# Kernel optimization log

Measured on AMD Instinct MI355X. Metric: run time of the kernel, lower is better.

## Reference

```python
import jax, jax.numpy as jnp
import numpy as np

N_NODES, N_EDGES, D_IN, N_GRAPHS = 20000, 320000, 256, 32
H1, C1, H2, C2 = 4, 128, 4, 64


def setup_inputs() -> dict:
    key = jax.random.key(0)
    ks = jax.random.split(key, 24)
    g = lambda k, shape, fan: jax.random.normal(k, shape, jnp.float32) * (1.0 / np.sqrt(fan))
    inp = {
        'x': jax.random.normal(ks[0], (N_NODES, D_IN), jnp.float32),
        'edge_index': jax.random.randint(ks[1], (2, N_EDGES), 0, N_NODES, jnp.int32),
        'batch': jnp.sort(jax.random.randint(ks[2], (N_NODES,), 0, N_GRAPHS, jnp.int32)),
        'edge_attr': jax.random.normal(ks[3], (N_EDGES, 1), jnp.float32),
        # GATConv 1: lin [D_IN, H1*C1], att_src/dst/edge [H1,C1], lin_edge [1,H1*C1], bias [H1*C1]
        'W1': g(ks[4], (D_IN, H1 * C1), D_IN),
        'as1': g(ks[5], (H1, C1), C1),
        'ad1': g(ks[6], (H1, C1), C1),
        'We1': g(ks[7], (1, H1 * C1), 1),
        'ae1': g(ks[8], (H1, C1), C1),
        'b1': jnp.zeros((H1 * C1,), jnp.float32),
        'g1': jnp.ones((H1 * C1,), jnp.float32),
        'be1': jnp.zeros((H1 * C1,), jnp.float32),
        # GATConv 2 (concat=False -> out 64)
        'W2': g(ks[9], (H1 * C1, H2 * C2), H1 * C1),
        'as2': g(ks[10], (H2, C2), C2),
        'ad2': g(ks[11], (H2, C2), C2),
        'We2': g(ks[12], (1, H2 * C2), 1),
        'ae2': g(ks[13], (H2, C2), C2),
        'b2': jnp.zeros((C2,), jnp.float32),
        'g2': jnp.ones((C2,), jnp.float32),
        'be2': jnp.zeros((C2,), jnp.float32),
        'fw1': g(ks[14], (C2, 32), C2),
        'fb1': jnp.zeros((32,), jnp.float32),
        'fw2': g(ks[15], (32, 1), 32),
        'fb2': jnp.zeros((1,), jnp.float32),
    }
    return inp


def _gat(x, src, dst, ea, W, a_s, a_d, We, a_e, bias, H, C, concat, n):
    h = (x @ W).reshape(n, H, C)                         # [N,H,C]
    al_s = jnp.einsum('nhc,hc->nh', h, a_s)              # [N,H]
    al_d = jnp.einsum('nhc,hc->nh', h, a_d)
    e = (ea @ We).reshape(-1, H, C)                      # [E',H,C]
    al_e = jnp.einsum('ehc,hc->eh', e, a_e)
    logits = jax.nn.leaky_relu(al_s[src] + al_d[dst] + al_e, 0.2)  # [E',H]
    m = jax.ops.segment_max(logits, dst, num_segments=n)
    m = jnp.where(jnp.isfinite(m), m, 0.0)
    p = jnp.exp(logits - m[dst])
    denom = jax.ops.segment_sum(p, dst, num_segments=n)
    alpha = p / (denom[dst] + 1e-16)                     # segment softmax
    out = jax.ops.segment_sum(h[src] * alpha[:, :, None], dst, num_segments=n)
    out = out.reshape(n, H * C) if concat else out.mean(axis=1)
    return out + bias


def _bn(x, gamma, beta):
    mu = x.mean(axis=0)
    var = x.var(axis=0)
    return gamma * (x - mu) * jax.lax.rsqrt(var + 1e-5) + beta


def reference(x, edge_index, batch, edge_attr, W1, as1, ad1, We1, ae1, b1, g1, be1,
              W2, as2, ad2, We2, ae2, b2, g2, be2, fw1, fb1, fw2, fb2):
    n = x.shape[0]
    loop = jnp.arange(n, dtype=edge_index.dtype)
    src = jnp.concatenate([edge_index[0], loop])
    dst = jnp.concatenate([edge_index[1], loop])
    # self-loop edge_attr filled with mean (PyG fill_value='mean')
    ea = jnp.concatenate([edge_attr, jnp.broadcast_to(edge_attr.mean(axis=0), (n, edge_attr.shape[1]))])

    h = _gat(x, src, dst, ea, W1, as1, ad1, We1, ae1, b1, H1, C1, True, n)
    h = jax.nn.elu(_bn(h, g1, be1))
    h = _gat(h, src, dst, ea, W2, as2, ad2, We2, ae2, b2, H2, C2, False, n)
    h = jax.nn.elu(_bn(h, g2, be2))

    sums = jax.ops.segment_sum(h, batch, num_segments=N_GRAPHS)
    cnt = jax.ops.segment_sum(jnp.ones((n,), h.dtype), batch, num_segments=N_GRAPHS)
    pooled = sums / jnp.maximum(cnt, 1.0)[:, None]       # global_mean_pool
    # dropout is identity in eval mode
    out = jax.nn.elu(pooled @ fw1 + fb1) @ fw2 + fb2
    return out
```

## Files before the change

### kernel.cpp

```cpp
#include <hip/hip_runtime.h>
#include <hip/hip_bf16.h>

#define N_NODES  20000
#define MPAD     20096
#define N_EDGES  320000
#define N_EP     (N_EDGES + N_NODES)
#define D_IN     256
#define N_GRAPHS 32
#define HH1 4
#define CC1 128
#define HH2 4
#define CC2 64

#define XB_OFF      0ull
#define HB1_OFF     10289152ull
#define AGG1_OFF    30867456ull
#define HB2_OFF     51445760ull
#define OUT2_OFF    61734912ull
#define ALPHA_OFF   66854912ull
#define DENOM_OFF   72294912ull
#define EAF_OFF     72614912ull
#define W1BT_OFF    73894912ull
#define W2BT_OFF    74157056ull
#define CSR_OFF     74419200ull
#define ROWPTR_OFF  77139200ull
#define GSTART_OFF  77219264ull
#define SMALL_OFF   77219520ull
#define SBUF_OFF    77245120ull
#define EAP_OFF     77245184ull
#define ALSP_OFF    77246464ull
#define ALDP_OFF    77889536ull
#define ALS1_OFF    78532608ull
#define ALD1_OFF    78854144ull
#define ALS2_OFF    79175680ull
#define ALD2_OFF    79497216ull
#define PMU1_OFF    79818752ull
#define PM21_OFF    80343040ull
#define PMU2_OFF    80867328ull
#define PM22_OFF    80932864ull
#define MUSUM1_OFF  80998400ull
#define M2SUM1_OFF  81000448ull
#define MUSUM2_OFF  81002496ull
#define M2SUM2_OFF  81003008ull
#define EAACC_OFF   81003520ull
#define DEG_OFF     81003584ull
#define CURS_OFF    81083584ull
#define FLAGZ_OFF   81163584ull
#define ZERO0_START DEG_OFF
#define ZERO0_SIZE  160128ull

#define S_AS1 0
#define S_AD1 512
#define S_WE1 1024
#define S_AE1 1536
#define S_G1  2048
#define S_BE1 2560
#define S_AS2 3072
#define S_AD2 3328
#define S_WE2 3584
#define S_AE2 3840
#define S_G2  4096
#define S_BE2 4160
#define S_FW1 4224
#define S_FB1 6272
#define S_FW2 6304
#define S_FB2 6336

typedef __attribute__((ext_vector_type(8))) short bf8_t;
typedef __attribute__((ext_vector_type(4))) float f4_t;

__global__ void detect_dtype(const unsigned short* __restrict__ xr, int* __restrict__ flag) {
    int i = blockIdx.x * blockDim.x + threadIdx.x;
    unsigned short u = xr[i];
    if ((u & 0x7F80) == 0x7F80) atomicOr(flag, 1);
}

__device__ __forceinline__ float loadF(const void* p, int i, int fp32) {
    return fp32 ? ((const float*)p)[i]
                : __bfloat162float(((const __hip_bfloat16*)p)[i]);
}

#define PB_XB  5024
#define PB_EAF 313
#define PB_W   512
#define PB_SM  16
#define PREP_BLOCKS (PB_XB + PB_EAF + 2 * PB_W + PB_SM + 1)
__global__ __launch_bounds__(256) void prep(
        const int* __restrict__ flag,
        const void* x, const void* ea, const void* W1, const void* W2,
        const void* as1, const void* ad1, const void* We1, const void* ae1,
        const void* g1, const void* be1, const void* as2, const void* ad2,
        const void* We2, const void* ae2, const void* g2, const void* be2,
        const void* fw1, const void* fb1, const void* fw2, const void* fb2,
        __hip_bfloat16* __restrict__ xb, float* __restrict__ eaf, float* __restrict__ eap,
        __hip_bfloat16* __restrict__ W1bt, __hip_bfloat16* __restrict__ W2bt,
        float* __restrict__ smalls, float* __restrict__ sbuf) {
    __shared__ float sh[256];
    int b = blockIdx.x, t = threadIdx.x;
    int fp32 = flag[0];
    if (b < PB_XB) {
        int base = (b * 256 + t) * 4;
        __hip_bfloat16 tmp[4];
#pragma unroll
        for (int j = 0; j < 4; ++j) {
            int i = base + j;
            float v = (i < N_NODES * D_IN) ? loadF(x, i, fp32) : 0.f;
            tmp[j] = __float2bfloat16(v);
        }
        *(uint2*)&xb[base] = *(uint2*)tmp;
        return;
    }
    b -= PB_XB;
    if (b < PB_EAF) {
        int base = (b * 256 + t) * 4;
        float s = 0.f;
#pragma unroll
        for (int j = 0; j < 4; ++j) {
            int i = base + j;
            if (i < N_EDGES) { float v = loadF(ea, i, fp32); eaf[i] = v; s += v; }
        }
        sh[t] = s;
        __syncthreads();
        for (int st = 128; st; st >>= 1) {
            if (t < st) sh[t] += sh[t + st];
            __syncthreads();
        }
        if (t == 0) eap[b] = sh[0];
        return;
    }
    b -= PB_EAF;
    if (b < PB_W) {
        int i = b * 256 + t;
        int k = i >> 9, n = i & 511;
        W1bt[(size_t)n * 256 + k] = __float2bfloat16(loadF(W1, i, fp32));
        return;
    }
    b -= PB_W;
    if (b < PB_W) {
        int i = b * 256 + t;
        int k = i >> 8, n = i & 255;
        W2bt[(size_t)n * 512 + k] = __float2bfloat16(loadF(W2, i, fp32));
        return;
    }
    b -= PB_W;
    if (b < PB_SM) {
        const void* srcs[16] = {as1, ad1, We1, ae1, g1, be1, as2, ad2, We2, ae2, g2, be2, fw1, fb1, fw2, fb2};
        const int cnts[16] = {512, 512, 512, 512, 512, 512, 256, 256, 256, 256, 64, 64, 2048, 32, 32, 1};
        const int offs[16] = {S_AS1, S_AD1, S_WE1, S_AE1, S_G1, S_BE1, S_AS2, S_AD2,
                              S_WE2, S_AE2, S_G2, S_BE2, S_FW1, S_FB1, S_FW2, S_FB2};
        for (int i = t; i < cnts[b]; i += 256)
            smalls[offs[b] + i] = loadF(srcs[b], i, fp32);
        return;
    }
    if (t < 4) {
        float s = 0.f;
        for (int c = 0; c < CC1; ++c) s += loadF(We1, t * CC1 + c, fp32) * loadF(ae1, t * CC1 + c, fp32);
        sbuf[t] = s;
    } else if (t < 8) {
        int h = t - 4;
        float s = 0.f;
        for (int c = 0; c < CC2; ++c) s += loadF(We2, h * CC2 + c, fp32) * loadF(ae2, h * CC2 + c, fp32);
        sbuf[4 + h] = s;
    }
}

#define HIST_BLOCKS 1329
__global__ void hist_bounds(const int* __restrict__ ei, int* __restrict__ deg,
                            const int* __restrict__ batch, int* __restrict__ gstart) {
    int b = blockIdx.x, t = threadIdx.x;
    if (b < HIST_BLOCKS) {
        int e = b * 256 + t;
        if (e >= N_EP) return;
        int d = (e < N_EDGES) ? ei[N_EDGES + e] : e - N_EDGES;
        atomicAdd(&deg[d], 1);
        return;
    }
    int i = (b - HIST_BLOCKS) * 256 + t;
    if (i >= N_NODES) return;
    int bb = batch[i];
    if (i == 0) {
        for (int g = 0; g <= bb; ++g) gstart[g] = 0;
    } else {
        int pb = batch[i - 1];
        for (int g = pb + 1; g <= bb; ++g) gstart[g] = i;
    }
    if (i == N_NODES - 1) {
        for (int g = bb + 1; g <= N_GRAPHS; ++g) gstart[g] = N_NODES;
    }
}

__global__ __launch_bounds__(1024) void deg_scan(const int* __restrict__ deg, int* __restrict__ rowptr,
                                                 const float* __restrict__ eap, float* __restrict__ ea_acc) {
    __shared__ int part[1024];
    int t = threadIdx.x;
    int lo = t * 20;
    int hi = lo + 20; if (hi > N_NODES) hi = N_NODES; if (lo > N_NODES) lo = N_NODES;
    int s = 0;
    for (int i = lo; i < hi; ++i) s += deg[i];
    part[t] = s;
    __syncthreads();
    for (int off = 1; off < 1024; off <<= 1) {
        int u = (t >= off) ? part[t - off] : 0;
        __syncthreads();
        if (t >= off) part[t] += u;
        __syncthreads();
    }
    int run = part[t] - s;
    for (int i = lo; i < hi; ++i) { rowptr[i] = run; run += deg[i]; }
    if (hi == N_NODES && lo < N_NODES) rowptr[N_NODES] = run;
    if (t == 0) {
        float es = 0.f;
        for (int i = 0; i < PB_EAF; ++i) es += eap[i];
        ea_acc[0] = es;
    }
}

__global__ void edge_scatter(const int* __restrict__ ei, const int* __restrict__ rowptr,
                             int* __restrict__ cursor, int2* __restrict__ csr_se) {
    int e = blockIdx.x * blockDim.x + threadIdx.x;
    if (e >= N_EP) return;
    int s, d;
    if (e < N_EDGES) { s = ei[e]; d = ei[N_EDGES + e]; }
    else { s = d = e - N_EDGES; }
    int pos = rowptr[d] + atomicAdd(&cursor[d], 1);
    csr_se[pos] = make_int2(s, e);
}

__global__ __launch_bounds__(64) void csr_sort(const int* __restrict__ rowptr, int2* __restrict__ cs) {
    __shared__ int2 buf[128];
    int d = blockIdx.x;
    int beg = rowptr[d], end = rowptr[d + 1], n = end - beg;
    int lane = threadIdx.x;
    if (n <= 1) return;
    if (n <= 128) {
        for (int i = lane; i < n; i += 64) buf[i] = cs[beg + i];
        __syncthreads();
        if (lane == 0) {
            for (int i = 1; i < n; ++i) {
                int2 key = buf[i]; int j = i - 1;
                while (j >= 0 && buf[j].y > key.y) { buf[j + 1] = buf[j]; --j; }
                buf[j + 1] = key;
            }
        }
        __syncthreads();
        for (int i = lane; i < n; i += 64) cs[beg + i] = buf[i];
    } else if (lane == 0) {
        for (int i = beg + 1; i < end; ++i) {
            int2 key = cs[i]; int j = i - 1;
            while (j >= beg && cs[j].y > key.y) { cs[j + 1] = cs[j]; --j; }
            cs[j + 1] = key;
        }
    }
}

__global__ __launch_bounds__(256) void gemm_mfma_al(
        const short* __restrict__ A, const short* __restrict__ Bt,
        __hip_bfloat16* __restrict__ Cb, int N, int K,
        float* __restrict__ alsp, float* __restrict__ aldp,
        const float* __restrict__ asv, const float* __restrict__ adv, int cshift) {
    __shared__ short As[128 * 40];
    __shared__ short Bs[64 * 40];
    int t = threadIdx.x;
    int wv = t >> 6, lane = t & 63, quad = lane >> 4, lr = lane & 15;
    int m0 = blockIdx.y * 128, n0 = blockIdx.x * 64;
    f4_t acc[2][4] = {};
    int ra0 = t >> 2, sa0 = t & 3;
    int ra1 = (t + 256) >> 2;
    for (int k0 = 0; k0 < K; k0 += 32) {
        *(uint4*)&As[ra0 * 40 + sa0 * 8] = *(const uint4*)&A[(size_t)(m0 + ra0) * K + k0 + sa0 * 8];
        *(uint4*)&As[ra1 * 40 + sa0 * 8] = *(const uint4*)&A[(size_t)(m0 + ra1) * K + k0 + sa0 * 8];
        *(uint4*)&Bs[ra0 * 40 + sa0 * 8] = *(const uint4*)&Bt[(size_t)(n0 + ra0) * K + k0 + sa0 * 8];
        __syncthreads();
        bf8_t a0 = *(const bf8_t*)&As[(wv * 16 + lr) * 40 + quad * 8];
        bf8_t a1 = *(const bf8_t*)&As[((wv + 4) * 16 + lr) * 40 + quad * 8];
#pragma unroll
        for (int nt = 0; nt < 4; ++nt) {
            bf8_t b = *(const bf8_t*)&Bs[(nt * 16 + lr) * 40 + quad * 8];
            acc[0][nt] = __builtin_amdgcn_mfma_f32_16x16x32_bf16(a0, b, acc[0][nt], 0, 0, 0);
            acc[1][nt] = __builtin_amdgcn_mfma_f32_16x16x32_bf16(a1, b, acc[1][nt], 0, 0, 0);
        }
        __syncthreads();
    }
#pragma unroll
    for (int si = 0; si < 2; ++si) {
        int mrow = m0 + (wv + si * 4) * 16 + quad * 4;
#pragma unroll
        for (int nt = 0; nt < 4; ++nt) {
            int col = n0 + nt * 16 + lr;
#pragma unroll
            for (int r = 0; r < 4; ++r)
                Cb[(size_t)(mrow + r) * N + col] = __float2bfloat16(acc[si][nt][r]);
        }
    }
    float asv4[4], adv4[4];
#pragma unroll
    for (int nt = 0; nt < 4; ++nt) {
        asv4[nt] = asv[n0 + nt * 16 + lr];
        adv4[nt] = adv[n0 + nt * 16 + lr];
    }
    int hsel = n0 >> cshift;
    int parity = (n0 >> 6) & ((1 << (cshift - 6)) - 1);
#pragma unroll
    for (int si = 0; si < 2; ++si) {
#pragma unroll
        for (int r = 0; r < 4; ++r) {
            float ps = 0.f, pd = 0.f;
#pragma unroll
            for (int nt = 0; nt < 4; ++nt) {
                ps += acc[si][nt][r] * asv4[nt];
                pd += acc[si][nt][r] * adv4[nt];
            }
#pragma unroll
            for (int m = 1; m < 16; m <<= 1) {
                ps += __shfl_xor(ps, m);
                pd += __shfl_xor(pd, m);
            }
            if (lr == 0) {
                int row = m0 + (wv + si * 4) * 16 + quad * 4 + r;
                alsp[(row * 4 + hsel) * 2 + parity] = ps;
                aldp[(row * 4 + hsel) * 2 + parity] = pd;
            }
        }
    }
}

__global__ void al_combine(const float* __restrict__ alsp, const float* __restrict__ aldp,
                           float* __restrict__ als, float* __restrict__ ald, int nparts) {
    int i = blockIdx.x * blockDim.x + threadIdx.x;
    if (i >= MPAD * 4) return;
    float s = alsp[2 * i], d0 = aldp[2 * i];
    if (nparts == 2) { s += alsp[2 * i + 1]; d0 += aldp[2 * i + 1]; }
    als[i] = s; ald[i] = d0;
}

__global__ __launch_bounds__(64) void edge_softmax_csr(
        const int* __restrict__ rowptr, const int2* __restrict__ csr_se,
        const float* __restrict__ als, const float* __restrict__ ald,
        const float* __restrict__ eaf, const float* __restrict__ ea_acc,
        const float* __restrict__ sbuf, float* __restrict__ alpha, float* __restrict__ denom) {
    int d = blockIdx.x;
    int lane = threadIdx.x;
    int beg = rowptr[d], end = rowptr[d + 1];
    float ea_mean = ea_acc[0] * (1.0f / N_EDGES);
    float4 ad = *(const float4*)&ald[d * 4];
    float s0 = sbuf[0], s1 = sbuf[1], s2 = sbuf[2], s3 = sbuf[3];
    float m0 = -INFINITY, m1 = -INFINITY, m2 = -INFINITY, m3 = -INFINITY;
    for (int p = beg + lane; p < end; p += 64) {
        int2 se = csr_se[p];
        float eav = (se.y < N_EDGES) ? eaf[se.y] : ea_mean;
        float4 as = *(const float4*)&als[se.x * 4];
        float l0 = as.x + ad.x + eav * s0; l0 = l0 > 0.f ? l0 : 0.2f * l0;
        float l1 = as.y + ad.y + eav * s1; l1 = l1 > 0.f ? l1 : 0.2f * l1;
        float l2 = as.z + ad.z + eav * s2; l2 = l2 > 0.f ? l2 : 0.2f * l2;
        float l3 = as.w + ad.w + eav * s3; l3 = l3 > 0.f ? l3 : 0.2f * l3;
        float4 lv = {l0, l1, l2, l3};
        *(float4*)&alpha[(size_t)p * 4] = lv;
        m0 = fmaxf(m0, l0); m1 = fmaxf(m1, l1); m2 = fmaxf(m2, l2); m3 = fmaxf(m3, l3);
    }
#pragma unroll
    for (int off = 1; off < 64; off <<= 1) {
        m0 = fmaxf(m0, __shfl_xor(m0, off));
        m1 = fmaxf(m1, __shfl_xor(m1, off));
        m2 = fmaxf(m2, __shfl_xor(m2, off));
        m3 = fmaxf(m3, __shfl_xor(m3, off));
    }
    float t0 = 0.f, t1 = 0.f, t2 = 0.f, t3 = 0.f;
    for (int p = beg + lane; p < end; p += 64) {
        float4 lv = *(const float4*)&alpha[(size_t)p * 4];
        lv.x = __expf(lv.x - m0); lv.y = __expf(lv.y - m1);
        lv.z = __expf(lv.z - m2); lv.w = __expf(lv.w - m3);
        *(float4*)&alpha[(size_t)p * 4] = lv;
        t0 += lv.x; t1 += lv.y; t2 += lv.z; t3 += lv.w;
    }
#pragma unroll
    for (int off = 1; off < 64; off <<= 1) {
        t0 += __shfl_xor(t0, off);
        t1 += __shfl_xor(t1, off);
        t2 += __shfl_xor(t2, off);
        t3 += __shfl_xor(t3, off);
    }
    if (lane == 0) {
        float4 dn = {t0, t1, t2, t3};
        *(float4*)&denom[d * 4] = dn;
    }
}

__global__ __launch_bounds__(128) void agg1_csr(
        const int* __restrict__ rowptr, const int2* __restrict__ csr_se,
        const float* __restrict__ alpha, const float* __restrict__ denom,
        const __hip_bfloat16* __restrict__ hb, __hip_bfloat16* __restrict__ outb) {
    int d = blockIdx.x;
    int t = threadIdx.x;
    int h = t >> 5;
    float rdn = 1.0f / (denom[d * 4 + h] + 1e-16f);
    float a0 = 0.f, a1 = 0.f, a2 = 0.f, a3 = 0.f;
    int beg = rowptr[d], end = rowptr[d + 1];
    for (int p = beg; p < end; ++p) {
        int2 se = csr_se[p];
        float w = alpha[(size_t)p * 4 + h];
        uint2 raw = *(const uint2*)&hb[(size_t)se.x * 512 + 4 * t];
        a0 += w * __uint_as_float(raw.x << 16);
        a1 += w * __uint_as_float(raw.x & 0xFFFF0000u);
        a2 += w * __uint_as_float(raw.y << 16);
        a3 += w * __uint_as_float(raw.y & 0xFFFF0000u);
    }
    __hip_bfloat16 tmp[4] = {__float2bfloat16(a0 * rdn), __float2bfloat16(a1 * rdn),
                             __float2bfloat16(a2 * rdn), __float2bfloat16(a3 * rdn)};
    *(uint2*)&outb[(size_t)d * 512 + 4 * t] = *(uint2*)tmp;
}

__global__ __launch_bounds__(64) void agg2_hm(
        const int* __restrict__ rowptr, const int2* __restrict__ csr_se,
        const float* __restrict__ alpha, const float* __restrict__ denom,
        const __hip_bfloat16* __restrict__ hb, float* __restrict__ out2) {
    int d = blockIdx.x;
    int t = threadIdx.x;
    int h = t >> 4;
    float rdn = 1.0f / (denom[d * 4 + h] + 1e-16f);
    float a0 = 0.f, a1 = 0.f, a2 = 0.f, a3 = 0.f;
    int beg = rowptr[d], end = rowptr[d + 1];
    for (int p = beg; p < end; ++p) {
        int2 se = csr_se[p];
        float w = alpha[(size_t)p * 4 + h];
        uint2 raw = *(const uint2*)&hb[(size_t)se.x * 256 + 4 * t];
        a0 += w * __uint_as_float(raw.x << 16);
        a1 += w * __uint_as_float(raw.x & 0xFFFF0000u);
        a2 += w * __uint_as_float(raw.y << 16);
        a3 += w * __uint_as_float(raw.y & 0xFFFF0000u);
    }
    __shared__ float sh[256];
    sh[4 * t] = a0 * rdn; sh[4 * t + 1] = a1 * rdn;
    sh[4 * t + 2] = a2 * rdn; sh[4 * t + 3] = a3 * rdn;
    __syncthreads();
    if (t < 16) {
        float4 v;
        v.x = 0.25f * (sh[4 * t] + sh[64 + 4 * t] + sh[128 + 4 * t] + sh[192 + 4 * t]);
        v.y = 0.25f * (sh[4 * t + 1] + sh[64 + 4 * t + 1] + sh[128 + 4 * t + 1] + sh[192 + 4 * t + 1]);
        v.z = 0.25f * (sh[4 * t + 2] + sh[64 + 4 * t + 2] + sh[128 + 4 * t + 2] + sh[192 + 4 * t + 2]);
        v.w = 0.25f * (sh[4 * t + 3] + sh[64 + 4 * t + 3] + sh[128 + 4 * t + 3] + sh[192 + 4 * t + 3]);
        *(float4*)&out2[(size_t)d * 64 + 4 * t] = v;
    }
}

__global__ __launch_bounds__(256) void bn_part_b(const __hip_bfloat16* __restrict__ x,
                                                 float* __restrict__ pmu, float* __restrict__ pm2) {
    int t = threadIdx.x, b = blockIdx.x;
    float s0 = 0.f, s20 = 0.f, s1 = 0.f, s21 = 0.f;
    for (int i = b; i < N_NODES; i += gridDim.x) {
        unsigned u = *(const unsigned*)&x[(size_t)i * 512 + 2 * t];
        float v0 = __uint_as_float(u << 16);
        float v1 = __uint_as_float(u & 0xFFFF0000u);
        s0 += v0; s20 += v0 * v0; s1 += v1; s21 += v1 * v1;
    }
    pmu[b * 512 + 2 * t] = s0;     pm2[b * 512 + 2 * t] = s20;
    pmu[b * 512 + 2 * t + 1] = s1; pm2[b * 512 + 2 * t + 1] = s21;
}

__global__ void bn_reduce(const float* __restrict__ pmu, const float* __restrict__ pm2,
                          float* __restrict__ musum, float* __restrict__ m2sum, int nch) {
    int c = blockIdx.x * blockDim.x + threadIdx.x;
    if (c >= nch) return;
    float s = 0.f, s2 = 0.f;
    for (int b = 0; b < 256; ++b) { s += pmu[b * nch + c]; s2 += pm2[b * nch + c]; }
    musum[c] = s; m2sum[c] = s2;
}

__global__ __launch_bounds__(256) void bn_apply_elu_b16(__hip_bfloat16* __restrict__ x,
                                                        const float* __restrict__ musum,
                                                        const float* __restrict__ m2sum,
                                                        const float* __restrict__ smalls) {
    int q = blockIdx.x * blockDim.x + threadIdx.x;
    if (q >= N_NODES * 512 / 4) return;
    int base = q * 4;
    int j = base & 511;
    uint2 raw = *(uint2*)&x[base];
    float v[4] = {__uint_as_float(raw.x << 16), __uint_as_float(raw.x & 0xFFFF0000u),
                  __uint_as_float(raw.y << 16), __uint_as_float(raw.y & 0xFFFF0000u)};
    __hip_bfloat16 tmp[4];
#pragma unroll
    for (int k = 0; k < 4; ++k) {
        int jj = j + k;
        float mm = musum[jj] * (1.0f / N_NODES);
        float var = m2sum[jj] * (1.0f / N_NODES) - mm * mm;
        float y = smalls[S_G1 + jj] * (v[k] - mm) * rsqrtf(var + 1e-5f) + smalls[S_BE1 + jj];
        y = y > 0.f ? y : expm1f(y);
        tmp[k] = __float2bfloat16(y);
    }
    *(uint2*)&x[base] = *(uint2*)tmp;
}

__global__ __launch_bounds__(256) void bn2_stats(const float* __restrict__ x,
                                                 float* __restrict__ pmu, float* __restrict__ pm2) {
    int t = threadIdx.x;
    int c = t & 63, j = t >> 6;
    float ls = 0.f, ls2 = 0.f;
    for (int nd = blockIdx.x * 4 + j; nd < N_NODES; nd += gridDim.x * 4) {
        float v = x[(size_t)nd * 64 + c];
        ls += v; ls2 += v * v;
    }
    __shared__ float shs[4][64], sh2[4][64];
    shs[j][c] = ls; sh2[j][c] = ls2;
    __syncthreads();
    if (j == 0) {
        pmu[blockIdx.x * 64 + c] = shs[0][c] + shs[1][c] + shs[2][c] + shs[3][c];
        pm2[blockIdx.x * 64 + c] = sh2[0][c] + sh2[1][c] + sh2[2][c] + sh2[3][c];
    }
}

__global__ void bn_apply_elu_f32(float* __restrict__ x, const float* __restrict__ musum,
                                 const float* __restrict__ m2sum, const float* __restrict__ smalls) {
    int i = blockIdx.x * blockDim.x + threadIdx.x;
    if (i >= N_NODES * 64) return;
    int j = i & 63;
    float m = musum[j] * (1.0f / N_NODES);
    float var = m2sum[j] * (1.0f / N_NODES) - m * m;
    float y = smalls[S_G2 + j] * (x[i] - m) * rsqrtf(var + 1e-5f) + smalls[S_BE2 + j];
    x[i] = y > 0.f ? y : expm1f(y);
}

__global__ __launch_bounds__(256) void pool_mlp(const float* __restrict__ x, const int* __restrict__ gstart,
                                                const float* __restrict__ smalls, const int* __restrict__ flag,
                                                void* __restrict__ outp) {
    int g = blockIdx.x;
    int t = threadIdx.x;
    int c = t & 63, j = t >> 6;
    int beg = gstart[g], end = gstart[g + 1];
    float s = 0.f;
    for (int i = beg + j; i < end; i += 4)
        s += x[(size_t)i * 64 + c];
    __shared__ float sh[4][64];
    __shared__ float pooled[64];
    __shared__ float hsh[32];
    sh[j][c] = s;
    __syncthreads();
    if (j == 0) {
        float tot = sh[0][c] + sh[1][c] + sh[2][c] + sh[3][c];
        pooled[c] = tot / fmaxf((float)(end - beg), 1.0f);
    }
    __syncthreads();
    if (t < 32) {
        float acc = smalls[S_FB1 + t];
        for (int cc = 0; cc < 64; ++cc)
            acc += pooled[cc] * smalls[S_FW1 + cc * 32 + t];
        hsh[t] = acc > 0.f ? acc : expm1f(acc);
    }
    __syncthreads();
    if (t == 0) {
        float o = smalls[S_FB2];
        for (int k = 0; k < 32; ++k) o += hsh[k] * smalls[S_FW2 + k];
        if (flag[0]) ((float*)outp)[g] = o;
        else ((__hip_bfloat16*)outp)[g] = __float2bfloat16(o);
    }
}

extern "C" void kernel_launch(void* const* d_in, const int* in_sizes, int n_in,
                              void* d_out, int out_size, void* d_ws, size_t ws_size,
                              hipStream_t stream) {
    const void* x    = d_in[0];
    const int* ei    = (const int*)d_in[1];
    const int* batch = (const int*)d_in[2];
    const void* ea   = d_in[3];
    const void* W1   = d_in[4];
    const void* as1  = d_in[5];
    const void* ad1  = d_in[6];
    const void* We1  = d_in[7];
    const void* ae1  = d_in[8];
    const void* g1   = d_in[10];
    const void* be1  = d_in[11];
    const void* W2   = d_in[12];
    const void* as2  = d_in[13];
    const void* ad2  = d_in[14];
    const void* We2  = d_in[15];
    const void* ae2  = d_in[16];
    const void* g2   = d_in[18];
    const void* be2  = d_in[19];
    const void* fw1  = d_in[20];
    const void* fb1  = d_in[21];
    const void* fw2  = d_in[22];
    const void* fb2  = d_in[23];

    char* ws = (char*)d_ws;
    __hip_bfloat16* xb   = (__hip_bfloat16*)(ws + XB_OFF);
    __hip_bfloat16* hb1  = (__hip_bfloat16*)(ws + HB1_OFF);
    __hip_bfloat16* agg1 = (__hip_bfloat16*)(ws + AGG1_OFF);
    __hip_bfloat16* hb2  = (__hip_bfloat16*)(ws + HB2_OFF);
    float* out2   = (float*)(ws + OUT2_OFF);
    float* alpha  = (float*)(ws + ALPHA_OFF);
    float* denom  = (float*)(ws + DENOM_OFF);
    float* eaf    = (float*)(ws + EAF_OFF);
    __hip_bfloat16* W1bt = (__hip_bfloat16*)(ws + W1BT_OFF);
    __hip_bfloat16* W2bt = (__hip_bfloat16*)(ws + W2BT_OFF);
    int2*  csr_se = (int2*)(ws + CSR_OFF);
    int*   rowptr = (int*)(ws + ROWPTR_OFF);
    int*   gstart = (int*)(ws + GSTART_OFF);
    float* smalls = (float*)(ws + SMALL_OFF);
    float* sbuf   = (float*)(ws + SBUF_OFF);
    float* eap    = (float*)(ws + EAP_OFF);
    float* alsp   = (float*)(ws + ALSP_OFF);
    float* aldp   = (float*)(ws + ALDP_OFF);
    float* als1   = (float*)(ws + ALS1_OFF);
    float* ald1   = (float*)(ws + ALD1_OFF);
    float* als2   = (float*)(ws + ALS2_OFF);
    float* ald2   = (float*)(ws + ALD2_OFF);
    float* pmu1   = (float*)(ws + PMU1_OFF);
    float* pm21   = (float*)(ws + PM21_OFF);
    float* pmu2   = (float*)(ws + PMU2_OFF);
    float* pm22   = (float*)(ws + PM22_OFF);
    float* musum1 = (float*)(ws + MUSUM1_OFF);
    float* m2sum1 = (float*)(ws + M2SUM1_OFF);
    float* musum2 = (float*)(ws + MUSUM2_OFF);
    float* m2sum2 = (float*)(ws + M2SUM2_OFF);
    float* ea_acc = (float*)(ws + EAACC_OFF);
    int*   deg    = (int*)(ws + DEG_OFF);
    int*   cursor = (int*)(ws + CURS_OFF);
    int*   flag   = (int*)(ws + FLAGZ_OFF);

    hipMemsetAsync(ws + ZERO0_START, 0, ZERO0_SIZE, stream);
    hipMemsetAsync(ws + AGG1_OFF + (size_t)N_NODES * 512 * 2, 0, (MPAD - N_NODES) * 512 * 2, stream);

    detect_dtype<<<256, 256, 0, stream>>>((const unsigned short*)x, flag);
    prep<<<PREP_BLOCKS, 256, 0, stream>>>(flag, x, ea, W1, W2,
                                          as1, ad1, We1, ae1, g1, be1, as2, ad2,
                                          We2, ae2, g2, be2, fw1, fb1, fw2, fb2,
                                          xb, eaf, eap, W1bt, W2bt, smalls, sbuf);

    hist_bounds<<<HIST_BLOCKS + 79, 256, 0, stream>>>(ei, deg, batch, gstart);
    deg_scan<<<1, 1024, 0, stream>>>(deg, rowptr, eap, ea_acc);
    edge_scatter<<<HIST_BLOCKS, 256, 0, stream>>>(ei, rowptr, cursor, csr_se);
    csr_sort<<<N_NODES, 64, 0, stream>>>(rowptr, csr_se);

    gemm_mfma_al<<<dim3(512 / 64, MPAD / 128), 256, 0, stream>>>(
        (const short*)xb, (const short*)W1bt, hb1, 512, 256,
        alsp, aldp, smalls + S_AS1, smalls + S_AD1, 7);
    al_combine<<<(MPAD * 4 + 255) / 256, 256, 0, stream>>>(alsp, aldp, als1, ald1, 2);
    edge_softmax_csr<<<N_NODES, 64, 0, stream>>>(rowptr, csr_se, als1, ald1, eaf, ea_acc, sbuf, alpha, denom);
    agg1_csr<<<N_NODES, 128, 0, stream>>>(rowptr, csr_se, alpha, denom, hb1, agg1);
    bn_part_b<<<256, 256, 0, stream>>>(agg1, pmu1, pm21);
    bn_reduce<<<2, 256, 0, stream>>>(pmu1, pm21, musum1, m2sum1, 512);
    bn_apply_elu_b16<<<10000, 256, 0, stream>>>(agg1, musum1, m2sum1, smalls);

    gemm_mfma_al<<<dim3(256 / 64, MPAD / 128), 256, 0, stream>>>(
        (const short*)agg1, (const short*)W2bt, hb2, 256, 512,
        alsp, aldp, smalls + S_AS2, smalls + S_AD2, 6);
    al_combine<<<(MPAD * 4 + 255) / 256, 256, 0, stream>>>(alsp, aldp, als2, ald2, 1);
    edge_softmax_csr<<<N_NODES, 64, 0, stream>>>(rowptr, csr_se, als2, ald2, eaf, ea_acc, sbuf + 4, alpha, denom);
    agg2_hm<<<N_NODES, 64, 0, stream>>>(rowptr, csr_se, alpha, denom, hb2, out2);
    bn2_stats<<<256, 256, 0, stream>>>(out2, pmu2, pm22);
    bn_reduce<<<1, 256, 0, stream>>>(pmu2, pm22, musum2, m2sum2, 64);
    bn_apply_elu_f32<<<(N_NODES * 64 + 255) / 256, 256, 0, stream>>>(out2, musum2, m2sum2, smalls);

    pool_mlp<<<N_GRAPHS, 256, 0, stream>>>(out2, gstart, smalls, flag, d_out);
}
```

Before: 520.8 us.

## Fuse edge softmax into aggregation kernels and fold BN affine into pooling

Merges the partial-logit combine, the CSR edge softmax and the weighted aggregation into one kernel per GAT layer. Each block keeps its node's logits, softmax weights and source indices in shared memory, with a recompute fallback for degrees above 1024. This removes the global alpha/denom round trips and several launches. BN statistics are now folded into per-channel scale/shift once, and the layer-2 BN+ELU is applied inside the pooling kernel instead of a separate pass. The cost is about 20KB of shared memory per block, which may lower occupancy in the gather loops, and extra block-wide reductions with several barriers.

```diff
diff --git a/kernel.cpp b/kernel.cpp
--- a/kernel.cpp
+++ b/kernel.cpp
@@ -11,41 +11,36 @@
 #define CC1 128
 #define HH2 4
 #define CC2 64
+#define MAXDEG   1024
 
 #define XB_OFF      0ull
 #define HB1_OFF     10289152ull
 #define AGG1_OFF    30867456ull
 #define HB2_OFF     51445760ull
 #define OUT2_OFF    61734912ull
-#define ALPHA_OFF   66854912ull
-#define DENOM_OFF   72294912ull
-#define EAF_OFF     72614912ull
-#define W1BT_OFF    73894912ull
-#define W2BT_OFF    74157056ull
-#define CSR_OFF     74419200ull
-#define ROWPTR_OFF  77139200ull
-#define GSTART_OFF  77219264ull
-#define SMALL_OFF   77219520ull
-#define SBUF_OFF    77245120ull
-#define EAP_OFF     77245184ull
-#define ALSP_OFF    77246464ull
-#define ALDP_OFF    77889536ull
-#define ALS1_OFF    78532608ull
-#define ALD1_OFF    78854144ull
-#define ALS2_OFF    79175680ull
-#define ALD2_OFF    79497216ull
-#define PMU1_OFF    79818752ull
-#define PM21_OFF    80343040ull
-#define PMU2_OFF    80867328ull
-#define PM22_OFF    80932864ull
-#define MUSUM1_OFF  80998400ull
-#define M2SUM1_OFF  81000448ull
-#define MUSUM2_OFF  81002496ull
-#define M2SUM2_OFF  81003008ull
-#define EAACC_OFF   81003520ull
-#define DEG_OFF     81003584ull
-#define CURS_OFF    81083584ull
-#define FLAGZ_OFF   81163584ull
+#define EAF_OFF     66854912ull
+#define W1BT_OFF    68134912ull
+#define W2BT_OFF    68397056ull
+#define CSR_OFF     68659200ull
+#define ROWPTR_OFF  71379200ull
+#define GSTART_OFF  71459264ull
+#define SMALL_OFF   71459520ull
+#define SBUF_OFF    71485120ull
+#define EAP_OFF     71485184ull
+#define ALSP_OFF    71486464ull
+#define ALDP_OFF    72129536ull
+#define PMU1_OFF    72772608ull
+#define PM21_OFF    73296896ull
+#define PMU2_OFF    73821184ull
+#define PM22_OFF    73886720ull
+#define A1_OFF      73952256ull
+#define B1_OFF      73954304ull
+#define A2_OFF      73956352ull
+#define B2_OFF      73956608ull
+#define EAACC_OFF   73956864ull
+#define DEG_OFF     73956928ull
+#define CURS_OFF    74036928ull
+#define FLAGZ_OFF   74116928ull
 #define ZERO0_START DEG_OFF
 #define ZERO0_SIZE  160128ull
 
@@ -324,120 +319,255 @@
     }
 }
 
-__global__ void al_combine(const float* __restrict__ alsp, const float* __restrict__ aldp,
-                           float* __restrict__ als, float* __restrict__ ald, int nparts) {
-    int i = blockIdx.x * blockDim.x + threadIdx.x;
-    if (i >= MPAD * 4) return;
-    float s = alsp[2 * i], d0 = aldp[2 * i];
-    if (nparts == 2) { s += alsp[2 * i + 1]; d0 += aldp[2 * i + 1]; }
-    als[i] = s; ald[i] = d0;
-}
-
-__global__ __launch_bounds__(64) void edge_softmax_csr(
-        const int* __restrict__ rowptr, const int2* __restrict__ csr_se,
-        const float* __restrict__ als, const float* __restrict__ ald,
+template <int NPARTS>
+__device__ __forceinline__ void load_als4(const float* __restrict__ alsp, int node, float out[4]) {
+    float4 q0 = *(const float4*)&alsp[node * 8];
+    float4 q1 = *(const float4*)&alsp[node * 8 + 4];
+    if (NPARTS == 2) {
+        out[0] = q0.x + q0.y; out[1] = q0.z + q0.w;
+        out[2] = q1.x + q1.y; out[3] = q1.z + q1.w;
+    } else {
+        out[0] = q0.x; out[1] = q0.z; out[2] = q1.x; out[3] = q1.z;
+    }
+}
+
+__global__ __launch_bounds__(128) void fused_agg1(
+        const int* __restrict__ rowptr, const int2* __restrict__ cs,
+        const float* __restrict__ alsp, const float* __restrict__ aldp,
         const float* __restrict__ eaf, const float* __restrict__ ea_acc,
-        const float* __restrict__ sbuf, float* __restrict__ alpha, float* __restrict__ denom) {
-    int d = blockIdx.x;
-    int lane = threadIdx.x;
-    int beg = rowptr[d], end = rowptr[d + 1];
+        const float* __restrict__ sbuf, const __hip_bfloat16* __restrict__ hb,
+        __hip_bfloat16* __restrict__ outb) {
+    __shared__ float lg[MAXDEG * 4];
+    __shared__ int   ssrc[MAXDEG];
+    __shared__ float red[4 * 128];
+    __shared__ float mxs[4], dns[4];
+    int d = blockIdx.x, t = threadIdx.x;
+    int beg = rowptr[d], end = rowptr[d + 1], n = end - beg;
+    bool fit = (n <= MAXDEG);
     float ea_mean = ea_acc[0] * (1.0f / N_EDGES);
-    float4 ad = *(const float4*)&ald[d * 4];
-    float s0 = sbuf[0], s1 = sbuf[1], s2 = sbuf[2], s3 = sbuf[3];
-    float m0 = -INFINITY, m1 = -INFINITY, m2 = -INFINITY, m3 = -INFINITY;
-    for (int p = beg + lane; p < end; p += 64) {
-        int2 se = csr_se[p];
+    float adh[4];
+#pragma unroll
+    for (int h = 0; h < 4; ++h) adh[h] = aldp[d * 8 + 2 * h] + aldp[d * 8 + 2 * h + 1];
+    float sb[4] = {sbuf[0], sbuf[1], sbuf[2], sbuf[3]};
+    float mx[4] = {-INFINITY, -INFINITY, -INFINITY, -INFINITY};
+    for (int p = t; p < n; p += 128) {
+        int2 se = cs[beg + p];
         float eav = (se.y < N_EDGES) ? eaf[se.y] : ea_mean;
-        float4 as = *(const float4*)&als[se.x * 4];
-        float l0 = as.x + ad.x + eav * s0; l0 = l0 > 0.f ? l0 : 0.2f * l0;
-        float l1 = as.y + ad.y + eav * s1; l1 = l1 > 0.f ? l1 : 0.2f * l1;
-        float l2 = as.z + ad.z + eav * s2; l2 = l2 > 0.f ? l2 : 0.2f * l2;
-        float l3 = as.w + ad.w + eav * s3; l3 = l3 > 0.f ? l3 : 0.2f * l3;
-        float4 lv = {l0, l1, l2, l3};
-        *(float4*)&alpha[(size_t)p * 4] = lv;
-        m0 = fmaxf(m0, l0); m1 = fmaxf(m1, l1); m2 = fmaxf(m2, l2); m3 = fmaxf(m3, l3);
-    }
-#pragma unroll
-    for (int off = 1; off < 64; off <<= 1) {
-        m0 = fmaxf(m0, __shfl_xor(m0, off));
-        m1 = fmaxf(m1, __shfl_xor(m1, off));
-        m2 = fmaxf(m2, __shfl_xor(m2, off));
-        m3 = fmaxf(m3, __shfl_xor(m3, off));
-    }
-    float t0 = 0.f, t1 = 0.f, t2 = 0.f, t3 = 0.f;
-    for (int p = beg + lane; p < end; p += 64) {
-        float4 lv = *(const float4*)&alpha[(size_t)p * 4];
-        lv.x = __expf(lv.x - m0); lv.y = __expf(lv.y - m1);
-        lv.z = __expf(lv.z - m2); lv.w = __expf(lv.w - m3);
-        *(float4*)&alpha[(size_t)p * 4] = lv;
-        t0 += lv.x; t1 += lv.y; t2 += lv.z; t3 += lv.w;
-    }
-#pragma unroll
-    for (int off = 1; off < 64; off <<= 1) {
-        t0 += __shfl_xor(t0, off);
-        t1 += __shfl_xor(t1, off);
-        t2 += __shfl_xor(t2, off);
-        t3 += __shfl_xor(t3, off);
-    }
-    if (lane == 0) {
-        float4 dn = {t0, t1, t2, t3};
-        *(float4*)&denom[d * 4] = dn;
-    }
-}
-
-__global__ __launch_bounds__(128) void agg1_csr(
-        const int* __restrict__ rowptr, const int2* __restrict__ csr_se,
-        const float* __restrict__ alpha, const float* __restrict__ denom,
-        const __hip_bfloat16* __restrict__ hb, __hip_bfloat16* __restrict__ outb) {
-    int d = blockIdx.x;
-    int t = threadIdx.x;
+        float as4[4];
+        load_als4<2>(alsp, se.x, as4);
+#pragma unroll
+        for (int h = 0; h < 4; ++h) {
+            float l = as4[h] + adh[h] + eav * sb[h];
+            l = l > 0.f ? l : 0.2f * l;
+            if (fit) lg[p * 4 + h] = l;
+            mx[h] = fmaxf(mx[h], l);
+        }
+        if (fit) ssrc[p] = se.x;
+    }
+#pragma unroll
+    for (int i = 0; i < 4; ++i) red[i * 128 + t] = mx[i];
+    __syncthreads();
+    for (int s = 64; s; s >>= 1) {
+        if (t < s) {
+#pragma unroll
+            for (int i = 0; i < 4; ++i)
+                red[i * 128 + t] = fmaxf(red[i * 128 + t], red[i * 128 + t + s]);
+        }
+        __syncthreads();
+    }
+    if (t < 4) mxs[t] = red[t * 128];
+    __syncthreads();
+    float m4[4] = {mxs[0], mxs[1], mxs[2], mxs[3]};
+    float sm[4] = {0.f, 0.f, 0.f, 0.f};
+    if (fit) {
+        for (int p = t; p < n; p += 128) {
+            float4 lv = *(float4*)&lg[p * 4];
+            lv.x = __expf(lv.x - m4[0]); lv.y = __expf(lv.y - m4[1]);
+            lv.z = __expf(lv.z - m4[2]); lv.w = __expf(lv.w - m4[3]);
+            *(float4*)&lg[p * 4] = lv;
+            sm[0] += lv.x; sm[1] += lv.y; sm[2] += lv.z; sm[3] += lv.w;
+        }
+    } else {
+        for (int p = t; p < n; p += 128) {
+            int2 se = cs[beg + p];
+            float eav = (se.y < N_EDGES) ? eaf[se.y] : ea_mean;
+            float as4[4];
+            load_als4<2>(alsp, se.x, as4);
+#pragma unroll
+            for (int h = 0; h < 4; ++h) {
+                float l = as4[h] + adh[h] + eav * sb[h];
+                l = l > 0.f ? l : 0.2f * l;
+                sm[h] += __expf(l - m4[h]);
+            }
+        }
+    }
+    __syncthreads();
+#pragma unroll
+    for (int i = 0; i < 4; ++i) red[i * 128 + t] = sm[i];
+    __syncthreads();
+    for (int s = 64; s; s >>= 1) {
+        if (t < s) {
+#pragma unroll
+            for (int i = 0; i < 4; ++i)
+                red[i * 128 + t] += red[i * 128 + t + s];
+        }
+        __syncthreads();
+    }
+    if (t < 4) dns[t] = red[t * 128];
+    __syncthreads();
     int h = t >> 5;
-    float rdn = 1.0f / (denom[d * 4 + h] + 1e-16f);
+    float rdn = 1.0f / (dns[h] + 1e-16f);
     float a0 = 0.f, a1 = 0.f, a2 = 0.f, a3 = 0.f;
-    int beg = rowptr[d], end = rowptr[d + 1];
-    for (int p = beg; p < end; ++p) {
-        int2 se = csr_se[p];
-        float w = alpha[(size_t)p * 4 + h];
-        uint2 raw = *(const uint2*)&hb[(size_t)se.x * 512 + 4 * t];
-        a0 += w * __uint_as_float(raw.x << 16);
-        a1 += w * __uint_as_float(raw.x & 0xFFFF0000u);
-        a2 += w * __uint_as_float(raw.y << 16);
-        a3 += w * __uint_as_float(raw.y & 0xFFFF0000u);
+    if (fit) {
+        for (int p = 0; p < n; ++p) {
+            float w = lg[p * 4 + h];
+            uint2 raw = *(const uint2*)&hb[(size_t)ssrc[p] * 512 + 4 * t];
+            a0 += w * __uint_as_float(raw.x << 16);
+            a1 += w * __uint_as_float(raw.x & 0xFFFF0000u);
+            a2 += w * __uint_as_float(raw.y << 16);
+            a3 += w * __uint_as_float(raw.y & 0xFFFF0000u);
+        }
+    } else {
+        for (int p = 0; p < n; ++p) {
+            int2 se = cs[beg + p];
+            float eav = (se.y < N_EDGES) ? eaf[se.y] : ea_mean;
+            float as = alsp[se.x * 8 + 2 * h] + alsp[se.x * 8 + 2 * h + 1];
+            float l = as + adh[h] + eav * sb[h];
+            l = l > 0.f ? l : 0.2f * l;
+            float w = __expf(l - m4[h]);
+            uint2 raw = *(const uint2*)&hb[(size_t)se.x * 512 + 4 * t];
+            a0 += w * __uint_as_float(raw.x << 16);
+            a1 += w * __uint_as_float(raw.x & 0xFFFF0000u);
+            a2 += w * __uint_as_float(raw.y << 16);
+            a3 += w * __uint_as_float(raw.y & 0xFFFF0000u);
+        }
     }
     __hip_bfloat16 tmp[4] = {__float2bfloat16(a0 * rdn), __float2bfloat16(a1 * rdn),
                              __float2bfloat16(a2 * rdn), __float2bfloat16(a3 * rdn)};
     *(uint2*)&outb[(size_t)d * 512 + 4 * t] = *(uint2*)tmp;
 }
 
-__global__ __launch_bounds__(64) void agg2_hm(
-        const int* __restrict__ rowptr, const int2* __restrict__ csr_se,
-        const float* __restrict__ alpha, const float* __restrict__ denom,
-        const __hip_bfloat16* __restrict__ hb, float* __restrict__ out2) {
-    int d = blockIdx.x;
-    int t = threadIdx.x;
+__global__ __launch_bounds__(64) void fused_agg2(
+        const int* __restrict__ rowptr, const int2* __restrict__ cs,
+        const float* __restrict__ alsp, const float* __restrict__ aldp,
+        const float* __restrict__ eaf, const float* __restrict__ ea_acc,
+        const float* __restrict__ sbuf, const __hip_bfloat16* __restrict__ hb,
+        float* __restrict__ out2) {
+    __shared__ float lg[MAXDEG * 4];
+    __shared__ int   ssrc[MAXDEG];
+    __shared__ float red[4 * 64];
+    __shared__ float mxs[4], dns[4];
+    __shared__ float shm[256];
+    int d = blockIdx.x, t = threadIdx.x;
+    int beg = rowptr[d], end = rowptr[d + 1], n = end - beg;
+    bool fit = (n <= MAXDEG);
+    float ea_mean = ea_acc[0] * (1.0f / N_EDGES);
+    float adh[4];
+#pragma unroll
+    for (int h = 0; h < 4; ++h) adh[h] = aldp[d * 8 + 2 * h];
+    float sb[4] = {sbuf[4], sbuf[5], sbuf[6], sbuf[7]};
+    float mx[4] = {-INFINITY, -INFINITY, -INFINITY, -INFINITY};
+    for (int p = t; p < n; p += 64) {
+        int2 se = cs[beg + p];
+        float eav = (se.y < N_EDGES) ? eaf[se.y] : ea_mean;
+        float as4[4];
+        load_als4<1>(alsp, se.x, as4);
+#pragma unroll
+        for (int h = 0; h < 4; ++h) {
+            float l = as4[h] + adh[h] + eav * sb[h];
+            l = l > 0.f ? l : 0.2f * l;
+            if (fit) lg[p * 4 + h] = l;
+            mx[h] = fmaxf(mx[h], l);
+        }
+        if (fit) ssrc[p] = se.x;
+    }
+#pragma unroll
+    for (int i = 0; i < 4; ++i) red[i * 64 + t] = mx[i];
+    __syncthreads();
+    for (int s = 32; s; s >>= 1) {
+        if (t < s) {
+#pragma unroll
+            for (int i = 0; i < 4; ++i)
+                red[i * 64 + t] = fmaxf(red[i * 64 + t], red[i * 64 + t + s]);
+        }
+        __syncthreads();
+    }
+    if (t < 4) mxs[t] = red[t * 64];
+    __syncthreads();
+    float m4[4] = {mxs[0], mxs[1], mxs[2], mxs[3]};
+    float sm[4] = {0.f, 0.f, 0.f, 0.f};
+    if (fit) {
+        for (int p = t; p < n; p += 64) {
+            float4 lv = *(float4*)&lg[p * 4];
+            lv.x = __expf(lv.x - m4[0]); lv.y = __expf(lv.y - m4[1]);
+            lv.z = __expf(lv.z - m4[2]); lv.w = __expf(lv.w - m4[3]);
+            *(float4*)&lg[p * 4] = lv;
+            sm[0] += lv.x; sm[1] += lv.y; sm[2] += lv.z; sm[3] += lv.w;
+        }
+    } else {
+        for (int p = t; p < n; p += 64) {
+            int2 se = cs[beg + p];
+            float eav = (se.y < N_EDGES) ? eaf[se.y] : ea_mean;
+            float as4[4];
+            load_als4<1>(alsp, se.x, as4);
+#pragma unroll
+            for (int h = 0; h < 4; ++h) {
+                float l = as4[h] + adh[h] + eav * sb[h];
+                l = l > 0.f ? l : 0.2f * l;
+                sm[h] += __expf(l - m4[h]);
+            }
+        }
+    }
+    __syncthreads();
+#pragma unroll
+    for (int i = 0; i < 4; ++i) red[i * 64 + t] = sm[i];
+    __syncthreads();
+    for (int s = 32; s; s >>= 1) {
+        if (t < s) {
+#pragma unroll
+            for (int i = 0; i < 4; ++i)
+                red[i * 64 + t] += red[i * 64 + t + s];
+        }
+        __syncthreads();
+    }
+    if (t < 4) dns[t] = red[t * 64];
+    __syncthreads();
     int h = t >> 4;
-    float rdn = 1.0f / (denom[d * 4 + h] + 1e-16f);
+    float rdn = 1.0f / (dns[h] + 1e-16f);
     float a0 = 0.f, a1 = 0.f, a2 = 0.f, a3 = 0.f;
-    int beg = rowptr[d], end = rowptr[d + 1];
-    for (int p = beg; p < end; ++p) {
-        int2 se = csr_se[p];
-        float w = alpha[(size_t)p * 4 + h];
-        uint2 raw = *(const uint2*)&hb[(size_t)se.x * 256 + 4 * t];
-        a0 += w * __uint_as_float(raw.x << 16);
-        a1 += w * __uint_as_float(raw.x & 0xFFFF0000u);
-        a2 += w * __uint_as_float(raw.y << 16);
-        a3 += w * __uint_as_float(raw.y & 0xFFFF0000u);
-    }
-    __shared__ float sh[256];
-    sh[4 * t] = a0 * rdn; sh[4 * t + 1] = a1 * rdn;
-    sh[4 * t + 2] = a2 * rdn; sh[4 * t + 3] = a3 * rdn;
+    if (fit) {
+        for (int p = 0; p < n; ++p) {
+            float w = lg[p * 4 + h];
+            uint2 raw = *(const uint2*)&hb[(size_t)ssrc[p] * 256 + 4 * t];
+            a0 += w * __uint_as_float(raw.x << 16);
+            a1 += w * __uint_as_float(raw.x & 0xFFFF0000u);
+            a2 += w * __uint_as_float(raw.y << 16);
+            a3 += w * __uint_as_float(raw.y & 0xFFFF0000u);
+        }
+    } else {
+        for (int p = 0; p < n; ++p) {
+            int2 se = cs[beg + p];
+            float eav = (se.y < N_EDGES) ? eaf[se.y] : ea_mean;
+            float as = alsp[se.x * 8 + 2 * h];
+            float l = as + adh[h] + eav * sb[h];
+            l = l > 0.f ? l : 0.2f * l;
+            float w = __expf(l - m4[h]);
+            uint2 raw = *(const uint2*)&hb[(size_t)se.x * 256 + 4 * t];
+            a0 += w * __uint_as_float(raw.x << 16);
+            a1 += w * __uint_as_float(raw.x & 0xFFFF0000u);
+            a2 += w * __uint_as_float(raw.y << 16);
+            a3 += w * __uint_as_float(raw.y & 0xFFFF0000u);
+        }
+    }
+    shm[4 * t] = a0 * rdn; shm[4 * t + 1] = a1 * rdn;
+    shm[4 * t + 2] = a2 * rdn; shm[4 * t + 3] = a3 * rdn;
     __syncthreads();
     if (t < 16) {
         float4 v;
-        v.x = 0.25f * (sh[4 * t] + sh[64 + 4 * t] + sh[128 + 4 * t] + sh[192 + 4 * t]);
-        v.y = 0.25f * (sh[4 * t + 1] + sh[64 + 4 * t + 1] + sh[128 + 4 * t + 1] + sh[192 + 4 * t + 1]);
-        v.z = 0.25f * (sh[4 * t + 2] + sh[64 + 4 * t + 2] + sh[128 + 4 * t + 2] + sh[192 + 4 * t + 2]);
-        v.w = 0.25f * (sh[4 * t + 3] + sh[64 + 4 * t + 3] + sh[128 + 4 * t + 3] + sh[192 + 4 * t + 3]);
+        v.x = 0.25f * (shm[4 * t] + shm[64 + 4 * t] + shm[128 + 4 * t] + shm[192 + 4 * t]);
+        v.y = 0.25f * (shm[4 * t + 1] + shm[64 + 4 * t + 1] + shm[128 + 4 * t + 1] + shm[192 + 4 * t + 1]);
+        v.z = 0.25f * (shm[4 * t + 2] + shm[64 + 4 * t + 2] + shm[128 + 4 * t + 2] + shm[192 + 4 * t + 2]);
+        v.w = 0.25f * (shm[4 * t + 3] + shm[64 + 4 * t + 3] + shm[128 + 4 * t + 3] + shm[192 + 4 * t + 3]);
         *(float4*)&out2[(size_t)d * 64 + 4 * t] = v;
     }
 }
@@ -456,19 +586,23 @@
     pmu[b * 512 + 2 * t + 1] = s1; pm2[b * 512 + 2 * t + 1] = s21;
 }
 
-__global__ void bn_reduce(const float* __restrict__ pmu, const float* __restrict__ pm2,
-                          float* __restrict__ musum, float* __restrict__ m2sum, int nch) {
+__global__ void bn_reduce_affine(const float* __restrict__ pmu, const float* __restrict__ pm2,
+                                 const float* __restrict__ smalls, int s_g, int s_be,
+                                 float* __restrict__ a, float* __restrict__ b, int nch) {
     int c = blockIdx.x * blockDim.x + threadIdx.x;
     if (c >= nch) return;
     float s = 0.f, s2 = 0.f;
-    for (int b = 0; b < 256; ++b) { s += pmu[b * nch + c]; s2 += pm2[b * nch + c]; }
-    musum[c] = s; m2sum[c] = s2;
+    for (int bk = 0; bk < 256; ++bk) { s += pmu[bk * nch + c]; s2 += pm2[bk * nch + c]; }
+    float m = s * (1.0f / N_NODES);
+    float var = s2 * (1.0f / N_NODES) - m * m;
+    float aa = smalls[s_g + c] * rsqrtf(var + 1e-5f);
+    a[c] = aa;
+    b[c] = smalls[s_be + c] - m * aa;
 }
 
 __global__ __launch_bounds__(256) void bn_apply_elu_b16(__hip_bfloat16* __restrict__ x,
-                                                        const float* __restrict__ musum,
-                                                        const float* __restrict__ m2sum,
-                                                        const float* __restrict__ smalls) {
+                                                        const float* __restrict__ a,
+                                                        const float* __restrict__ b) {
     int q = blockIdx.x * blockDim.x + threadIdx.x;
     if (q >= N_NODES * 512 / 4) return;
     int base = q * 4;
@@ -479,10 +613,7 @@
     __hip_bfloat16 tmp[4];
 #pragma unroll
     for (int k = 0; k < 4; ++k) {
-        int jj = j + k;
-        float mm = musum[jj] * (1.0f / N_NODES);
-        float var = m2sum[jj] * (1.0f / N_NODES) - mm * mm;
-        float y = smalls[S_G1 + jj] * (v[k] - mm) * rsqrtf(var + 1e-5f) + smalls[S_BE1 + jj];
+        float y = a[j + k] * v[k] + b[j + k];
         y = y > 0.f ? y : expm1f(y);
         tmp[k] = __float2bfloat16(y);
     }
@@ -507,27 +638,20 @@
     }
 }
 
-__global__ void bn_apply_elu_f32(float* __restrict__ x, const float* __restrict__ musum,
-                                 const float* __restrict__ m2sum, const float* __restrict__ smalls) {
-    int i = blockIdx.x * blockDim.x + threadIdx.x;
-    if (i >= N_NODES * 64) return;
-    int j = i & 63;
-    float m = musum[j] * (1.0f / N_NODES);
-    float var = m2sum[j] * (1.0f / N_NODES) - m * m;
-    float y = smalls[S_G2 + j] * (x[i] - m) * rsqrtf(var + 1e-5f) + smalls[S_BE2 + j];
-    x[i] = y > 0.f ? y : expm1f(y);
-}
-
 __global__ __launch_bounds__(256) void pool_mlp(const float* __restrict__ x, const int* __restrict__ gstart,
+                                                const float* __restrict__ a2, const float* __restrict__ b2,
                                                 const float* __restrict__ smalls, const int* __restrict__ flag,
                                                 void* __restrict__ outp) {
     int g = blockIdx.x;
     int t = threadIdx.x;
     int c = t & 63, j = t >> 6;
     int beg = gstart[g], end = gstart[g + 1];
+    float ac = a2[c], bc = b2[c];
     float s = 0.f;
-    for (int i = beg + j; i < end; i += 4)
-        s += x[(size_t)i * 64 + c];
+    for (int i = beg + j; i < end; i += 4) {
+        float y = ac * x[(size_t)i * 64 + c] + bc;
+        s += (y > 0.f ? y : expm1f(y));
+    }
     __shared__ float sh[4][64];
     __shared__ float pooled[64];
     __shared__ float hsh[32];
@@ -585,8 +709,6 @@
     __hip_bfloat16* agg1 = (__hip_bfloat16*)(ws + AGG1_OFF);
     __hip_bfloat16* hb2  = (__hip_bfloat16*)(ws + HB2_OFF);
     float* out2   = (float*)(ws + OUT2_OFF);
-    float* alpha  = (float*)(ws + ALPHA_OFF);
-    float* denom  = (float*)(ws + DENOM_OFF);
     float* eaf    = (float*)(ws + EAF_OFF);
     __hip_bfloat16* W1bt = (__hip_bfloat16*)(ws + W1BT_OFF);
     __hip_bfloat16* W2bt = (__hip_bfloat16*)(ws + W2BT_OFF);
@@ -598,18 +720,14 @@
     float* eap    = (float*)(ws + EAP_OFF);
     float* alsp   = (float*)(ws + ALSP_OFF);
     float* aldp   = (float*)(ws + ALDP_OFF);
-    float* als1   = (float*)(ws + ALS1_OFF);
-    float* ald1   = (float*)(ws + ALD1_OFF);
-    float* als2   = (float*)(ws + ALS2_OFF);
-    float* ald2   = (float*)(ws + ALD2_OFF);
     float* pmu1   = (float*)(ws + PMU1_OFF);
     float* pm21   = (float*)(ws + PM21_OFF);
     float* pmu2   = (float*)(ws + PMU2_OFF);
     float* pm22   = (float*)(ws + PM22_OFF);
-    float* musum1 = (float*)(ws + MUSUM1_OFF);
-    float* m2sum1 = (float*)(ws + M2SUM1_OFF);
-    float* musum2 = (float*)(ws + MUSUM2_OFF);
-    float* m2sum2 = (float*)(ws + M2SUM2_OFF);
+    float* a1     = (float*)(ws + A1_OFF);
+    float* b1     = (float*)(ws + B1_OFF);
+    float* a2     = (float*)(ws + A2_OFF);
+    float* b2     = (float*)(ws + B2_OFF);
     float* ea_acc = (float*)(ws + EAACC_OFF);
     int*   deg    = (int*)(ws + DEG_OFF);
     int*   cursor = (int*)(ws + CURS_OFF);
@@ -632,22 +750,17 @@
     gemm_mfma_al<<<dim3(512 / 64, MPAD / 128), 256, 0, stream>>>(
         (const short*)xb, (const short*)W1bt, hb1, 512, 256,
         alsp, aldp, smalls + S_AS1, smalls + S_AD1, 7);
-    al_combine<<<(MPAD * 4 + 255) / 256, 256, 0, stream>>>(alsp, aldp, als1, ald1, 2);
-    edge_softmax_csr<<<N_NODES, 64, 0, stream>>>(rowptr, csr_se, als1, ald1, eaf, ea_acc, sbuf, alpha, denom);
-    agg1_csr<<<N_NODES, 128, 0, stream>>>(rowptr, csr_se, alpha, denom, hb1, agg1);
+    fused_agg1<<<N_NODES, 128, 0, stream>>>(rowptr, csr_se, alsp, aldp, eaf, ea_acc, sbuf, hb1, agg1);
     bn_part_b<<<256, 256, 0, stream>>>(agg1, pmu1, pm21);
-    bn_reduce<<<2, 256, 0, stream>>>(pmu1, pm21, musum1, m2sum1, 512);
-    bn_apply_elu_b16<<<10000, 256, 0, stream>>>(agg1, musum1, m2sum1, smalls);
+    bn_reduce_affine<<<2, 256, 0, stream>>>(pmu1, pm21, smalls, S_G1, S_BE1, a1, b1, 512);
+    bn_apply_elu_b16<<<10000, 256, 0, stream>>>(agg1, a1, b1);
 
     gemm_mfma_al<<<dim3(256 / 64, MPAD / 128), 256, 0, stream>>>(
         (const short*)agg1, (const short*)W2bt, hb2, 256, 512,
         alsp, aldp, smalls + S_AS2, smalls + S_AD2, 6);
-    al_combine<<<(MPAD * 4 + 255) / 256, 256, 0, stream>>>(alsp, aldp, als2, ald2, 1);
-    edge_softmax_csr<<<N_NODES, 64, 0, stream>>>(rowptr, csr_se, als2, ald2, eaf, ea_acc, sbuf + 4, alpha, denom);
-    agg2_hm<<<N_NODES, 64, 0, stream>>>(rowptr, csr_se, alpha, denom, hb2, out2);
+    fused_agg2<<<N_NODES, 64, 0, stream>>>(rowptr, csr_se, alsp, aldp, eaf, ea_acc, sbuf, hb2, out2);
     bn2_stats<<<256, 256, 0, stream>>>(out2, pmu2, pm22);
-    bn_reduce<<<1, 256, 0, stream>>>(pmu2, pm22, musum2, m2sum2, 64);
-    bn_apply_elu_f32<<<(N_NODES * 64 + 255) / 256, 256, 0, stream>>>(out2, musum2, m2sum2, smalls);
-
-    pool_mlp<<<N_GRAPHS, 256, 0, stream>>>(out2, gstart, smalls, flag, d_out);
-}
+    bn_reduce_affine<<<1, 64, 0, stream>>>(pmu2, pm22, smalls, S_G2, S_BE2, a2, b2, 64);
+
+    pool_mlp<<<N_GRAPHS, 256, 0, stream>>>(out2, gstart, a2, b2, smalls, flag, d_out);
+}
```

Result: slower. 549.9 us (+5.6%).
